# Optimization experiments

Hardware: AMD Instinct MI355X
Metric: run time of the kernel (lower is better)

## Reference

```python
import jax, jax.numpy as jnp
import numpy as np

C = 64

def setup_inputs() -> dict:
    key = jax.random.key(0)
    ks = jax.random.split(key, 8)
    B, H, W = 4, 64, 64
    s = 1.0 / np.sqrt(C)
    return {
        "x": jax.random.normal(ks[0], (B, C, H, W), dtype=jnp.float32),
        "ln_g": jnp.ones((C,), jnp.float32),
        "ln_b": jnp.zeros((C,), jnp.float32),
        "wq": jax.random.normal(ks[1], (C, C), jnp.float32) * s,
        "bq": jnp.zeros((C,), jnp.float32),
        "wk": jax.random.normal(ks[2], (C, 1, 3, 3), jnp.float32) / 3.0,
        "bk": jnp.zeros((C,), jnp.float32),
        "wv": jax.random.normal(ks[3], (C, 1, 3, 3), jnp.float32) / 3.0,
        "bv": jnp.zeros((C,), jnp.float32),
        "wo": jax.random.normal(ks[4], (C, C), jnp.float32) * s,
        "bo": jnp.zeros((C,), jnp.float32),
    }

def _dwconv3x3(x, w, b):
    # depthwise 3x3, padding=1, groups=C; x: (B,C,H,W), w: (C,1,3,3)
    y = jax.lax.conv_general_dilated(
        x, w, window_strides=(1, 1), padding="SAME",
        feature_group_count=x.shape[1],
        dimension_numbers=("NCHW", "OIHW", "NCHW"))
    return y + b[None, :, None, None]

def reference(x, ln_g, ln_b, wq, bq, wk, bk, wv, bv, wo, bo):
    B, Cc, H, W = x.shape
    scale = jnp.sqrt(jnp.asarray(Cc, x.dtype))
    # LayerNorm over channel dim (torch LayerNorm([C]) on (B,H,W,C))
    mu = jnp.mean(x, axis=1, keepdims=True)
    var = jnp.mean(jnp.square(x - mu), axis=1, keepdims=True)
    xn = (x - mu) / jnp.sqrt(var + 1e-5)
    xn = xn * ln_g[None, :, None, None] + ln_b[None, :, None, None]
    # projections
    q = jnp.einsum("oc,bchw->bohw", wq, xn) + bq[None, :, None, None]
    k = _dwconv3x3(xn, wk, bk)
    v = _dwconv3x3(xn, wv, bv)
    HW = H * W
    qf = q.reshape(B, Cc, HW)  # (B,C,N)
    kf = k.reshape(B, Cc, HW)
    vf = v.reshape(B, Cc, HW)
    # attn[b,i,j] = sum_c q[b,c,i] k[b,c,j] / sqrt(C)
    attn = jnp.einsum("bci,bcj->bij", qf, kf) / scale
    attn = jax.nn.softmax(attn, axis=-1)
    # out[b,c,i] = sum_j attn[b,i,j] v[b,c,j]
    out = jnp.einsum("bij,bcj->bci", attn, vf).reshape(B, Cc, H, W)
    out = jnp.einsum("oc,bchw->bohw", wo, out) + bo[None, :, None, None]
    return out + x
```

## Files before the change

kernel.cpp:

```cpp
#include <hip/hip_runtime.h>
#include <stdint.h>

typedef __attribute__((ext_vector_type(8))) short short8;
typedef __attribute__((ext_vector_type(4))) float f32x4;

#define MFMA16(A, B, C) __builtin_amdgcn_mfma_f32_16x16x32_bf16(A, B, C, 0, 0, 0)

__device__ __forceinline__ short f2bf(float f) {
    uint32_t u = __float_as_uint(f);
    u = (u + 0x7fffu + ((u >> 16) & 1u)) >> 16;
    return (short)u;
}
__device__ __forceinline__ float bf2f(short s) {
    return __uint_as_float(((uint32_t)(uint16_t)s) << 16);
}
__device__ __forceinline__ uint32_t pk_bf_trunc(float a, float b) {
    return __builtin_amdgcn_perm(__float_as_uint(b), __float_as_uint(a), 0x07060302u);
}

__device__ __forceinline__ void async_cp16(void* lds, const void* gm) {
    __builtin_amdgcn_global_load_lds(
        (const __attribute__((address_space(1))) unsigned int*)gm,
        (__attribute__((address_space(3))) unsigned int*)lds,
        16, 0, 0);
}

__device__ __forceinline__ int swz(int row, int col) {
    return row * 64 + ((((col >> 3) ^ (row & 7)) << 3) | (col & 7));
}

__device__ __forceinline__ short8 ldg_f8_bf(const float* __restrict__ p) {
    float4 a = *(const float4*)p;
    float4 b = *(const float4*)(p + 4);
    short8 r;
    r[0] = f2bf(a.x); r[1] = f2bf(a.y); r[2] = f2bf(a.z); r[3] = f2bf(a.w);
    r[4] = f2bf(b.x); r[5] = f2bf(b.y); r[6] = f2bf(b.z); r[7] = f2bf(b.w);
    return r;
}

__global__ __launch_bounds__(512, 2) void k_lnqkv(
    const float* __restrict__ xg, const float* __restrict__ lng, const float* __restrict__ lnb,
    const float* __restrict__ wq, const float* __restrict__ bq,
    const float* __restrict__ wkg, const float* __restrict__ bk,
    const float* __restrict__ wvg, const float* __restrict__ bv,
    short* __restrict__ Qt, short* __restrict__ KVg)
{
    const int t    = threadIdx.x;
    const int wv   = t >> 6;
    const int lane = t & 63;
    const int l15  = lane & 15;
    const int quad = lane >> 4;
    const int h    = blockIdx.x;
    const int b    = blockIdx.y;

    __shared__ float xl[3 * 64 * 66];
    __shared__ short sb[64 * 72];
    __shared__ float wkl[576], wvl[576], bkl[64], bvl[64];

    float* muL = (float*)sb;
    float* rsL = muL + 192;

    float rv[24];
    #pragma unroll
    for (int k = 0; k < 24; ++k) {
        int idx = t + (k << 9);
        int dy = idx >> 12, rem = idx & 4095;
        int c = rem >> 6, w = rem & 63;
        int hh = h + dy - 1;
        rv[k] = 0.f;
        if (hh >= 0 && hh < 64) rv[k] = xg[((b * 64 + c) * 64 + hh) * 64 + w];
    }
    for (int idx = t; idx < 576; idx += 512) { wkl[idx] = wkg[idx]; wvl[idx] = wvg[idx]; }
    if (t < 64) { bkl[t] = bk[t]; bvl[t] = bv[t]; }
    #pragma unroll
    for (int k = 0; k < 24; ++k) {
        int idx = t + (k << 9);
        int dy = idx >> 12, rem = idx & 4095;
        int c = rem >> 6, w = rem & 63;
        xl[(dy * 64 + c) * 66 + w] = rv[k];
    }
    __syncthreads();

    if (t < 384) {
        int dy = t >> 7;
        int rem = t & 127;
        int w = rem >> 1, half = rem & 1;
        const float* col = &xl[(dy * 64 + half * 32) * 66 + w];
        float s = 0.f, ss = 0.f;
        #pragma unroll
        for (int cc = 0; cc < 32; ++cc) {
            float v = col[cc * 66];
            s += v; ss = fmaf(v, v, ss);
        }
        s  += __shfl_xor(s, 1);
        ss += __shfl_xor(ss, 1);
        if (half == 0) {
            float mu  = s * (1.f / 64.f);
            float var = ss * (1.f / 64.f) - mu * mu;
            muL[dy * 64 + w] = mu;
            rsL[dy * 64 + w] = rsqrtf(var + 1e-5f);
        }
    }
    __syncthreads();

    #pragma unroll
    for (int k = 0; k < 24; ++k) {
        int idx = t + (k << 9);
        int dy = idx >> 12, rem = idx & 4095;
        int c = rem >> 6, w = rem & 63;
        int hh = h + dy - 1;
        float v = xl[(dy * 64 + c) * 66 + w];
        int p = dy * 64 + w;
        v = (v - muL[p]) * rsL[p] * lng[c] + lnb[c];
        if (hh < 0 || hh >= 64) v = 0.f;
        xl[(dy * 64 + c) * 66 + w] = v;
    }
    __syncthreads();

    {
        short* xnt = sb;
        int c = t & 63;
        #pragma unroll
        for (int k = 0; k < 8; ++k) {
            int w = wv + (k << 3);
            xnt[w * 72 + c] = f2bf(xl[(64 + c) * 66 + w]);
        }
    }
    __syncthreads();

    {
        const short* xnt = sb;
        const int tile = wv >> 1, half = wv & 1;
        short8 af[2];
        #pragma unroll
        for (int kc = 0; kc < 2; ++kc)
            af[kc] = *(const short8*)&xnt[(tile * 16 + l15) * 72 + kc * 32 + quad * 8];
        f32x4 acc[2];
        acc[0] = (f32x4){0.f, 0.f, 0.f, 0.f};
        acc[1] = (f32x4){0.f, 0.f, 0.f, 0.f};
        #pragma unroll
        for (int kc = 0; kc < 2; ++kc) {
            #pragma unroll
            for (int ntl = 0; ntl < 2; ++ntl) {
                int nt = half * 2 + ntl;
                short8 bf = ldg_f8_bf(&wq[(nt * 16 + l15) * 64 + kc * 32 + quad * 8]);
                acc[ntl] = MFMA16(af[kc], bf, acc[ntl]);
            }
        }
        const float c1 = 0.18033688011112042f;
        #pragma unroll
        for (int ntl = 0; ntl < 2; ++ntl) {
            int o = (half * 2 + ntl) * 16 + l15;
            float bqv = bq[o];
            #pragma unroll
            for (int r = 0; r < 4; ++r) {
                int w = tile * 16 + quad * 4 + r;
                Qt[((b * 4096 + h * 64 + w) << 6) + o] = f2bf((acc[ntl][r] + bqv) * c1);
            }
        }
    }
    __syncthreads();

    {
        short* vt = sb;
        int c  = t & 63;
        int w0 = wv << 3;
        float wk9[9], wv9[9];
        #pragma unroll
        for (int q = 0; q < 9; ++q) { wk9[q] = wkl[c * 9 + q]; wv9[q] = wvl[c * 9 + q]; }
        float acck[8], accv[8];
        #pragma unroll
        for (int j = 0; j < 8; ++j) { acck[j] = bkl[c]; accv[j] = bvl[c]; }
        #pragma unroll
        for (int dy = 0; dy < 3; ++dy) {
            const float* row = &xl[(dy * 64 + c) * 66];
            float r[10];
            r[0] = (w0 == 0) ? 0.f : row[w0 - 1];
            #pragma unroll
            for (int j = 0; j < 8; ++j) r[j + 1] = row[w0 + j];
            r[9] = (w0 == 56) ? 0.f : row[w0 + 8];
            #pragma unroll
            for (int j = 0; j < 8; ++j) {
                acck[j] += wk9[0 + dy * 3] * r[j] + wk9[1 + dy * 3] * r[j + 1] + wk9[2 + dy * 3] * r[j + 2];
                accv[j] += wv9[0 + dy * 3] * r[j] + wv9[1 + dy * 3] * r[j + 1] + wv9[2 + dy * 3] * r[j + 2];
            }
        }
        long tb = (long)(b * 64 + h) * 8192;
        #pragma unroll
        for (int j = 0; j < 8; ++j)
            KVg[tb + swz(w0 + j, c)] = f2bf(acck[j]);
        #pragma unroll
        for (int j = 0; j < 8; ++j)
            vt[c * 72 + w0 + j] = f2bf(accv[j]);
    }
    __syncthreads();

    {
        const short* vt = sb;
        long tb = (long)(b * 64 + h) * 8192 + 4096;
        for (int idx = t; idx < 4096; idx += 512) {
            int c = idx >> 6, jl = idx & 63;
            int s = ((jl & 15) << 2) | (jl >> 4);
            KVg[tb + swz(c, s)] = vt[c * 72 + jl];
        }
    }
}

__global__ __launch_bounds__(128, 2) void k_attn(
    const short* __restrict__ Qt, const short* __restrict__ KVg,
    short* __restrict__ Ogb, float* __restrict__ Lg)
{
    const int t    = threadIdx.x;
    const int wv   = t >> 6;
    const int lane = t & 63;
    const int l15  = lane & 15;
    const int quad = lane >> 4;
    const int ti   = blockIdx.x;
    const int jp   = blockIdx.y;
    const int b    = blockIdx.z;
    const int iw   = ti * 64 + wv * 32;

    __shared__ short kvb0[8192];
    __shared__ short kvb1[8192];
    __shared__ short ldsP[2 * 16 * 72];
    short* myP = &ldsP[wv * 16 * 72];

    const short* kvg = KVg + ((long)b * 64 + jp * 16) * 8192;

    short8 qf[2][2];
    #pragma unroll
    for (int rs = 0; rs < 2; ++rs)
        #pragma unroll
        for (int kc = 0; kc < 2; ++kc)
            qf[rs][kc] = *(const short8*)&Qt[((b * 4096 + iw + rs * 16 + l15) << 6) + kc * 32 + quad * 8];

    f32x4 oacc[2][4];
    #pragma unroll
    for (int rs = 0; rs < 2; ++rs)
        #pragma unroll
        for (int nt = 0; nt < 4; ++nt) oacc[rs][nt] = (f32x4){0.f, 0.f, 0.f, 0.f};
    float Lp[2][4] = {{0.f, 0.f, 0.f, 0.f}, {0.f, 0.f, 0.f, 0.f}};

    #pragma unroll
    for (int ii = 0; ii < 8; ++ii) {
        int inst = (wv << 3) + ii;
        async_cp16(kvb0 + inst * 512, kvg + inst * 512 + lane * 8);
    }

    const int xr = l15 & 7;

    #pragma unroll 1
    for (int jt = 0; jt < 16; ++jt) {
        short* cur = (jt & 1) ? kvb1 : kvb0;
        short* nxt = (jt & 1) ? kvb0 : kvb1;
        __syncthreads();
        if (jt < 15) {
            const short* g = kvg + (jt + 1) * 8192;
            #pragma unroll
            for (int ii = 0; ii < 8; ++ii) {
                int inst = (wv << 3) + ii;
                async_cp16(nxt + inst * 512, g + inst * 512 + lane * 8);
            }
        }

        short8 kf[4][2], vf[4][2];
        #pragma unroll
        for (int n = 0; n < 4; ++n) {
            int rbase = (n * 16 + l15) * 64;
            #pragma unroll
            for (int kc = 0; kc < 2; ++kc) {
                int cc = ((kc * 4 + quad) ^ xr) << 3;
                kf[n][kc] = *(const short8*)&cur[rbase + cc];
                vf[n][kc] = *(const short8*)&cur[4096 + rbase + cc];
            }
        }

        #pragma unroll
        for (int rs = 0; rs < 2; ++rs) {
            f32x4 sacc[4];
            #pragma unroll
            for (int n = 0; n < 4; ++n) sacc[n] = (f32x4){0.f, 0.f, 0.f, 0.f};
            #pragma unroll
            for (int kc = 0; kc < 2; ++kc)
                #pragma unroll
                for (int n = 0; n < 4; ++n)
                    sacc[n] = MFMA16(qf[rs][kc], kf[n][kc], sacc[n]);

            #pragma unroll
            for (int r = 0; r < 4; ++r) {
                float p0 = __builtin_amdgcn_exp2f(sacc[0][r]);
                float p1 = __builtin_amdgcn_exp2f(sacc[1][r]);
                float p2 = __builtin_amdgcn_exp2f(sacc[2][r]);
                float p3 = __builtin_amdgcn_exp2f(sacc[3][r]);
                Lp[rs][r] += (p0 + p1) + (p2 + p3);
                uint2 pk;
                pk.x = pk_bf_trunc(p0, p1);
                pk.y = pk_bf_trunc(p2, p3);
                *(uint2*)&myP[(quad * 4 + r) * 72 + l15 * 4] = pk;
            }
            short8 pf[2];
            #pragma unroll
            for (int kc = 0; kc < 2; ++kc)
                pf[kc] = *(const short8*)&myP[l15 * 72 + kc * 32 + quad * 8];
            #pragma unroll
            for (int kc = 0; kc < 2; ++kc)
                #pragma unroll
                for (int n = 0; n < 4; ++n)
                    oacc[rs][n] = MFMA16(pf[kc], vf[n][kc], oacc[rs][n]);
        }
    }

    const int p = b * 4 + jp;
    #pragma unroll
    for (int rs = 0; rs < 2; ++rs) {
        #pragma unroll
        for (int r = 0; r < 4; ++r) {
            #pragma unroll
            for (int off = 1; off < 16; off <<= 1)
                Lp[rs][r] += __shfl_xor(Lp[rs][r], off);
            int i = iw + rs * 16 + quad * 4 + r;
            if (l15 == 0) Lg[p * 4096 + i] = Lp[rs][r];
            #pragma unroll
            for (int nt = 0; nt < 4; ++nt)
                Ogb[((p * 4096 + i) << 6) + nt * 16 + l15] = f2bf(oacc[rs][nt][r]);
        }
    }
}

__global__ __launch_bounds__(256, 4) void k_out(
    const short* __restrict__ Ogb, const float* __restrict__ Lg,
    const float* __restrict__ wo, const float* __restrict__ bo,
    const float* __restrict__ xg, float* __restrict__ out)
{
    const int t    = threadIdx.x;
    const int wv4  = t >> 6;
    const int lane = t & 63;
    const int l15  = lane & 15;
    const int quad = lane >> 4;
    const int i0   = blockIdx.x * 16;
    const int b    = blockIdx.y;

    float Ls = 0.f;
    #pragma unroll
    for (int jp = 0; jp < 4; ++jp) Ls += Lg[(b * 4 + jp) * 4096 + i0 + l15];
    float invL = 1.0f / Ls;

    short8 af[2];
    #pragma unroll
    for (int kc = 0; kc < 2; ++kc)
        af[kc] = ldg_f8_bf(&wo[(wv4 * 16 + l15) * 64 + kc * 32 + quad * 8]);

    f32x4 acc = (f32x4){0.f, 0.f, 0.f, 0.f};
    #pragma unroll
    for (int kc = 0; kc < 2; ++kc) {
        float bs[8] = {0.f, 0.f, 0.f, 0.f, 0.f, 0.f, 0.f, 0.f};
        #pragma unroll
        for (int jp = 0; jp < 4; ++jp) {
            short8 ov = *(const short8*)&Ogb[(((b * 4 + jp) * 4096 + i0 + l15) << 6) + kc * 32 + quad * 8];
            #pragma unroll
            for (int e = 0; e < 8; ++e) bs[e] += bf2f(ov[e]);
        }
        short8 bfr;
        #pragma unroll
        for (int e = 0; e < 8; ++e) bfr[e] = f2bf(bs[e] * invL);
        acc = MFMA16(af[kc], bfr, acc);
    }
    #pragma unroll
    for (int r = 0; r < 4; ++r) {
        int o = wv4 * 16 + quad * 4 + r;
        long obase = ((long)(b * 64 + o)) << 12;
        out[obase + i0 + l15] = acc[r] + bo[o] + xg[obase + i0 + l15];
    }
}

extern "C" void kernel_launch(void* const* d_in, const int* in_sizes, int n_in,
                              void* d_out, int out_size, void* d_ws, size_t ws_size,
                              hipStream_t stream) {
    (void)in_sizes; (void)n_in; (void)out_size; (void)ws_size;
    const float* x   = (const float*)d_in[0];
    const float* lng = (const float*)d_in[1];
    const float* lnb = (const float*)d_in[2];
    const float* wq  = (const float*)d_in[3];
    const float* bq  = (const float*)d_in[4];
    const float* wk  = (const float*)d_in[5];
    const float* bk  = (const float*)d_in[6];
    const float* wvw = (const float*)d_in[7];
    const float* bv  = (const float*)d_in[8];
    const float* wo  = (const float*)d_in[9];
    const float* bo  = (const float*)d_in[10];
    float* out = (float*)d_out;

    short* Qt  = (short*)d_ws;
    short* KVg = Qt + 4 * 4096 * 64;
    short* Ogb = KVg + 4 * 64 * 8192;
    float* Lg  = (float*)(Ogb + 16 * 4096 * 64);

    k_lnqkv<<<dim3(64, 4), 512, 0, stream>>>(x, lng, lnb, wq, bq, wk, bk, wvw, bv, Qt, KVg);
    k_attn<<<dim3(64, 4, 4), 128, 0, stream>>>(Qt, KVg, Ogb, Lg);
    k_out<<<dim3(256, 4), 256, 0, stream>>>(Ogb, Lg, wo, bo, x, out);
}
```

Baseline: 118.8 us.

## Transpose attention MFMA so P stays in registers, double rows per wave

The attention kernel now computes S^T = K·Q^T, so the exponentiated probabilities come out in the register layout needed as the B operand of the PV MFMA. This removes the per-tile LDS round-trip for P. Each wave handles 64 query rows instead of 32, which halves the grid and doubles reuse of each K/V tile loaded into LDS, at the cost of more accumulator registers. The LN/QKV kernel also fuses the LayerNorm statistics into the global load pass, keeps normalized values in registers, and permutes V so its transposed store uses vectorized writes.

```diff
diff --git a/kernel.cpp b/kernel.cpp
--- a/kernel.cpp
+++ b/kernel.cpp
@@ -17,6 +17,7 @@
 __device__ __forceinline__ uint32_t pk_bf_trunc(float a, float b) {
     return __builtin_amdgcn_perm(__float_as_uint(b), __float_as_uint(a), 0x07060302u);
 }
+union PFU { uint32_t u[4]; short8 s; };
 
 __device__ __forceinline__ void async_cp16(void* lds, const void* gm) {
     __builtin_amdgcn_global_load_lds(
@@ -27,6 +28,9 @@
 
 __device__ __forceinline__ int swz(int row, int col) {
     return row * 64 + ((((col >> 3) ^ (row & 7)) << 3) | (col & 7));
+}
+__device__ __forceinline__ int pimap(int j) {
+    return ((j >> 5) << 5) + (((j >> 2) & 3) << 3) + (((j >> 4) & 1) << 2) + (j & 3);
 }
 
 __device__ __forceinline__ short8 ldg_f8_bf(const float* __restrict__ p) {
@@ -52,84 +56,74 @@
     const int quad = lane >> 4;
     const int h    = blockIdx.x;
     const int b    = blockIdx.y;
+    const int w    = t & 63;
+    const int g    = t >> 6;
 
     __shared__ float xl[3 * 64 * 66];
-    __shared__ short sb[64 * 72];
+    __shared__ float sfu[3072];
     __shared__ float wkl[576], wvl[576], bkl[64], bvl[64];
-
-    float* muL = (float*)sb;
-    float* rsL = muL + 192;
+    __shared__ float muL[192], rsL[192];
 
     float rv[24];
+    float s0 = 0.f, s1 = 0.f, s2 = 0.f, q0 = 0.f, q1 = 0.f, q2 = 0.f;
     #pragma unroll
     for (int k = 0; k < 24; ++k) {
-        int idx = t + (k << 9);
-        int dy = idx >> 12, rem = idx & 4095;
-        int c = rem >> 6, w = rem & 63;
-        int hh = h + dy - 1;
-        rv[k] = 0.f;
-        if (hh >= 0 && hh < 64) rv[k] = xg[((b * 64 + c) * 64 + hh) * 64 + w];
-    }
+        const int dy = k >> 3, c = g + 8 * (k & 7);
+        const int hh = h + dy - 1;
+        float v = 0.f;
+        if (hh >= 0 && hh < 64) v = xg[((b * 64 + c) * 64 + hh) * 64 + w];
+        rv[k] = v;
+        if (k < 8)       { s0 += v; q0 = fmaf(v, v, q0); }
+        else if (k < 16) { s1 += v; q1 = fmaf(v, v, q1); }
+        else             { s2 += v; q2 = fmaf(v, v, q2); }
+    }
+    float lngv[8], lnbv[8];
+    #pragma unroll
+    for (int j = 0; j < 8; ++j) { lngv[j] = lng[g + 8 * j]; lnbv[j] = lnb[g + 8 * j]; }
     for (int idx = t; idx < 576; idx += 512) { wkl[idx] = wkg[idx]; wvl[idx] = wvg[idx]; }
     if (t < 64) { bkl[t] = bk[t]; bvl[t] = bv[t]; }
     #pragma unroll
-    for (int k = 0; k < 24; ++k) {
-        int idx = t + (k << 9);
-        int dy = idx >> 12, rem = idx & 4095;
-        int c = rem >> 6, w = rem & 63;
-        xl[(dy * 64 + c) * 66 + w] = rv[k];
-    }
-    __syncthreads();
-
-    if (t < 384) {
-        int dy = t >> 7;
-        int rem = t & 127;
-        int w = rem >> 1, half = rem & 1;
-        const float* col = &xl[(dy * 64 + half * 32) * 66 + w];
-        float s = 0.f, ss = 0.f;
-        #pragma unroll
-        for (int cc = 0; cc < 32; ++cc) {
-            float v = col[cc * 66];
-            s += v; ss = fmaf(v, v, ss);
-        }
-        s  += __shfl_xor(s, 1);
-        ss += __shfl_xor(ss, 1);
-        if (half == 0) {
-            float mu  = s * (1.f / 64.f);
-            float var = ss * (1.f / 64.f) - mu * mu;
-            muL[dy * 64 + w] = mu;
-            rsL[dy * 64 + w] = rsqrtf(var + 1e-5f);
-        }
-    }
-    __syncthreads();
-
-    #pragma unroll
-    for (int k = 0; k < 24; ++k) {
-        int idx = t + (k << 9);
-        int dy = idx >> 12, rem = idx & 4095;
-        int c = rem >> 6, w = rem & 63;
-        int hh = h + dy - 1;
-        float v = xl[(dy * 64 + c) * 66 + w];
-        int p = dy * 64 + w;
-        v = (v - muL[p]) * rsL[p] * lng[c] + lnb[c];
-        if (hh < 0 || hh >= 64) v = 0.f;
-        xl[(dy * 64 + c) * 66 + w] = v;
-    }
-    __syncthreads();
-
+    for (int k = 0; k < 24; ++k)
+        xl[((k >> 3) * 64 + g + 8 * (k & 7)) * 66 + w] = rv[k];
+    sfu[(0 * 8 + g) * 64 + w] = s0; sfu[(1 * 8 + g) * 64 + w] = s1; sfu[(2 * 8 + g) * 64 + w] = s2;
+    sfu[1536 + (0 * 8 + g) * 64 + w] = q0; sfu[1536 + (1 * 8 + g) * 64 + w] = q1; sfu[1536 + (2 * 8 + g) * 64 + w] = q2;
+    __syncthreads();
+
+    if (t < 192) {
+        int dy = t >> 6, ww = t & 63;
+        float S = 0.f, SS = 0.f;
+        #pragma unroll
+        for (int gg = 0; gg < 8; ++gg) {
+            S  += sfu[(dy * 8 + gg) * 64 + ww];
+            SS += sfu[1536 + (dy * 8 + gg) * 64 + ww];
+        }
+        float mu  = S * (1.f / 64.f);
+        float var = SS * (1.f / 64.f) - mu * mu;
+        muL[t] = mu;
+        rsL[t] = rsqrtf(var + 1e-5f);
+    }
+    __syncthreads();
+
+    short* xnt = (short*)sfu;
     {
-        short* xnt = sb;
-        int c = t & 63;
-        #pragma unroll
-        for (int k = 0; k < 8; ++k) {
-            int w = wv + (k << 3);
-            xnt[w * 72 + c] = f2bf(xl[(64 + c) * 66 + w]);
+        float mua = muL[w], rsa = rsL[w];
+        float mub = muL[64 + w], rsb = rsL[64 + w];
+        float muc = muL[128 + w], rsc = rsL[128 + w];
+        #pragma unroll
+        for (int k = 0; k < 24; ++k) {
+            int dy = k >> 3, c = g + 8 * (k & 7);
+            int hh = h + dy - 1;
+            float mu = (k < 8) ? mua : (k < 16) ? mub : muc;
+            float rs = (k < 8) ? rsa : (k < 16) ? rsb : rsc;
+            float v = (rv[k] - mu) * rs * lngv[k & 7] + lnbv[k & 7];
+            if (hh < 0 || hh >= 64) v = 0.f;
+            xl[(dy * 64 + c) * 66 + w] = v;
+            if (dy == 1) xnt[w * 72 + c] = f2bf(v);
         }
     }
     __syncthreads();
 
     {
-        const short* xnt = sb;
         const int tile = wv >> 1, half = wv & 1;
         short8 af[2];
         #pragma unroll
@@ -154,15 +148,15 @@
             float bqv = bq[o];
             #pragma unroll
             for (int r = 0; r < 4; ++r) {
-                int w = tile * 16 + quad * 4 + r;
-                Qt[((b * 4096 + h * 64 + w) << 6) + o] = f2bf((acc[ntl][r] + bqv) * c1);
-            }
-        }
-    }
-    __syncthreads();
-
+                int ww = tile * 16 + quad * 4 + r;
+                Qt[((b * 4096 + h * 64 + ww) << 6) + o] = f2bf((acc[ntl][r] + bqv) * c1);
+            }
+        }
+    }
+    __syncthreads();
+
+    short* vt = (short*)sfu;
     {
-        short* vt = sb;
         int c  = t & 63;
         int w0 = wv << 3;
         float wk9[9], wv9[9];
@@ -177,12 +171,15 @@
             float r[10];
             r[0] = (w0 == 0) ? 0.f : row[w0 - 1];
             #pragma unroll
-            for (int j = 0; j < 8; ++j) r[j + 1] = row[w0 + j];
+            for (int j2 = 0; j2 < 4; ++j2) {
+                float2 p2 = *(const float2*)&row[w0 + j2 * 2];
+                r[1 + j2 * 2] = p2.x; r[2 + j2 * 2] = p2.y;
+            }
             r[9] = (w0 == 56) ? 0.f : row[w0 + 8];
             #pragma unroll
             for (int j = 0; j < 8; ++j) {
-                acck[j] += wk9[0 + dy * 3] * r[j] + wk9[1 + dy * 3] * r[j + 1] + wk9[2 + dy * 3] * r[j + 2];
-                accv[j] += wv9[0 + dy * 3] * r[j] + wv9[1 + dy * 3] * r[j + 1] + wv9[2 + dy * 3] * r[j + 2];
+                acck[j] += wk9[dy * 3] * r[j] + wk9[dy * 3 + 1] * r[j + 1] + wk9[dy * 3 + 2] * r[j + 2];
+                accv[j] += wv9[dy * 3] * r[j] + wv9[dy * 3 + 1] * r[j + 1] + wv9[dy * 3 + 2] * r[j + 2];
             }
         }
         long tb = (long)(b * 64 + h) * 8192;
@@ -191,17 +188,19 @@
             KVg[tb + swz(w0 + j, c)] = f2bf(acck[j]);
         #pragma unroll
         for (int j = 0; j < 8; ++j)
-            vt[c * 72 + w0 + j] = f2bf(accv[j]);
+            vt[c * 68 + pimap(w0 + j)] = f2bf(accv[j]);
     }
     __syncthreads();
 
     {
-        const short* vt = sb;
         long tb = (long)(b * 64 + h) * 8192 + 4096;
-        for (int idx = t; idx < 4096; idx += 512) {
-            int c = idx >> 6, jl = idx & 63;
-            int s = ((jl & 15) << 2) | (jl >> 4);
-            KVg[tb + swz(c, s)] = vt[c * 72 + jl];
+        #pragma unroll
+        for (int it = 0; it < 2; ++it) {
+            int grp = t + it * 512;
+            int c = grp >> 4, s0c = (grp & 15) * 4;
+            uint2 v = *(const uint2*)&vt[c * 68 + s0c];
+            int dst = c * 64 + ((((s0c >> 3) ^ (c & 7)) << 3) | (s0c & 7));
+            *(uint2*)&KVg[tb + dst] = v;
         }
     }
 }
@@ -218,34 +217,30 @@
     const int ti   = blockIdx.x;
     const int jp   = blockIdx.y;
     const int b    = blockIdx.z;
-    const int iw   = ti * 64 + wv * 32;
+    const int iw   = ti * 128 + wv * 64;
 
     __shared__ short kvb0[8192];
     __shared__ short kvb1[8192];
-    __shared__ short ldsP[2 * 16 * 72];
-    short* myP = &ldsP[wv * 16 * 72];
 
     const short* kvg = KVg + ((long)b * 64 + jp * 16) * 8192;
 
-    short8 qf[2][2];
-    #pragma unroll
-    for (int rs = 0; rs < 2; ++rs)
+    short8 qf[4][2];
+    #pragma unroll
+    for (int rs = 0; rs < 4; ++rs)
         #pragma unroll
         for (int kc = 0; kc < 2; ++kc)
             qf[rs][kc] = *(const short8*)&Qt[((b * 4096 + iw + rs * 16 + l15) << 6) + kc * 32 + quad * 8];
 
-    f32x4 oacc[2][4];
-    #pragma unroll
-    for (int rs = 0; rs < 2; ++rs)
-        #pragma unroll
-        for (int nt = 0; nt < 4; ++nt) oacc[rs][nt] = (f32x4){0.f, 0.f, 0.f, 0.f};
-    float Lp[2][4] = {{0.f, 0.f, 0.f, 0.f}, {0.f, 0.f, 0.f, 0.f}};
-
-    #pragma unroll
-    for (int ii = 0; ii < 8; ++ii) {
-        int inst = (wv << 3) + ii;
-        async_cp16(kvb0 + inst * 512, kvg + inst * 512 + lane * 8);
-    }
+    f32x4 oacc[4][4];
+    #pragma unroll
+    for (int rs = 0; rs < 4; ++rs)
+        #pragma unroll
+        for (int cb = 0; cb < 4; ++cb) oacc[rs][cb] = (f32x4){0.f, 0.f, 0.f, 0.f};
+    float Lp[4] = {0.f, 0.f, 0.f, 0.f};
+
+    #pragma unroll
+    for (int ii = 0; ii < 8; ++ii)
+        async_cp16(kvb0 + (wv * 8 + ii) * 512, kvg + (wv * 8 + ii) * 512 + lane * 8);
 
     const int xr = l15 & 7;
 
@@ -255,74 +250,68 @@
         short* nxt = (jt & 1) ? kvb0 : kvb1;
         __syncthreads();
         if (jt < 15) {
-            const short* g = kvg + (jt + 1) * 8192;
-            #pragma unroll
-            for (int ii = 0; ii < 8; ++ii) {
-                int inst = (wv << 3) + ii;
-                async_cp16(nxt + inst * 512, g + inst * 512 + lane * 8);
-            }
+            const short* gsrc = kvg + (jt + 1) * 8192;
+            #pragma unroll
+            for (int ii = 0; ii < 8; ++ii)
+                async_cp16(nxt + (wv * 8 + ii) * 512, gsrc + (wv * 8 + ii) * 512 + lane * 8);
         }
 
         short8 kf[4][2], vf[4][2];
         #pragma unroll
-        for (int n = 0; n < 4; ++n) {
-            int rbase = (n * 16 + l15) * 64;
+        for (int mb = 0; mb < 4; ++mb) {
+            int rbase = (mb * 16 + l15) * 64;
             #pragma unroll
             for (int kc = 0; kc < 2; ++kc) {
                 int cc = ((kc * 4 + quad) ^ xr) << 3;
-                kf[n][kc] = *(const short8*)&cur[rbase + cc];
-                vf[n][kc] = *(const short8*)&cur[4096 + rbase + cc];
-            }
-        }
-
-        #pragma unroll
-        for (int rs = 0; rs < 2; ++rs) {
+                kf[mb][kc] = *(const short8*)&cur[rbase + cc];
+                vf[mb][kc] = *(const short8*)&cur[4096 + rbase + cc];
+            }
+        }
+
+        #pragma unroll
+        for (int rs = 0; rs < 4; ++rs) {
             f32x4 sacc[4];
             #pragma unroll
-            for (int n = 0; n < 4; ++n) sacc[n] = (f32x4){0.f, 0.f, 0.f, 0.f};
+            for (int mb = 0; mb < 4; ++mb) sacc[mb] = (f32x4){0.f, 0.f, 0.f, 0.f};
             #pragma unroll
             for (int kc = 0; kc < 2; ++kc)
                 #pragma unroll
-                for (int n = 0; n < 4; ++n)
-                    sacc[n] = MFMA16(qf[rs][kc], kf[n][kc], sacc[n]);
-
-            #pragma unroll
-            for (int r = 0; r < 4; ++r) {
-                float p0 = __builtin_amdgcn_exp2f(sacc[0][r]);
-                float p1 = __builtin_amdgcn_exp2f(sacc[1][r]);
-                float p2 = __builtin_amdgcn_exp2f(sacc[2][r]);
-                float p3 = __builtin_amdgcn_exp2f(sacc[3][r]);
-                Lp[rs][r] += (p0 + p1) + (p2 + p3);
-                uint2 pk;
-                pk.x = pk_bf_trunc(p0, p1);
-                pk.y = pk_bf_trunc(p2, p3);
-                *(uint2*)&myP[(quad * 4 + r) * 72 + l15 * 4] = pk;
-            }
-            short8 pf[2];
-            #pragma unroll
-            for (int kc = 0; kc < 2; ++kc)
-                pf[kc] = *(const short8*)&myP[l15 * 72 + kc * 32 + quad * 8];
-            #pragma unroll
-            for (int kc = 0; kc < 2; ++kc)
+                for (int mb = 0; mb < 4; ++mb)
+                    sacc[mb] = MFMA16(kf[mb][kc], qf[rs][kc], sacc[mb]);
+
+            PFU pf[2];
+            #pragma unroll
+            for (int mb = 0; mb < 4; ++mb) {
+                float p0 = __builtin_amdgcn_exp2f(sacc[mb][0]);
+                float p1 = __builtin_amdgcn_exp2f(sacc[mb][1]);
+                float p2 = __builtin_amdgcn_exp2f(sacc[mb][2]);
+                float p3 = __builtin_amdgcn_exp2f(sacc[mb][3]);
+                Lp[rs] += (p0 + p1) + (p2 + p3);
+                pf[mb >> 1].u[(mb & 1) * 2 + 0] = pk_bf_trunc(p0, p1);
+                pf[mb >> 1].u[(mb & 1) * 2 + 1] = pk_bf_trunc(p2, p3);
+            }
+            #pragma unroll
+            for (int kcp = 0; kcp < 2; ++kcp)
                 #pragma unroll
-                for (int n = 0; n < 4; ++n)
-                    oacc[rs][n] = MFMA16(pf[kc], vf[n][kc], oacc[rs][n]);
+                for (int cb = 0; cb < 4; ++cb)
+                    oacc[rs][cb] = MFMA16(vf[cb][kcp], pf[kcp].s, oacc[rs][cb]);
         }
     }
 
     const int p = b * 4 + jp;
     #pragma unroll
-    for (int rs = 0; rs < 2; ++rs) {
-        #pragma unroll
-        for (int r = 0; r < 4; ++r) {
-            #pragma unroll
-            for (int off = 1; off < 16; off <<= 1)
-                Lp[rs][r] += __shfl_xor(Lp[rs][r], off);
-            int i = iw + rs * 16 + quad * 4 + r;
-            if (l15 == 0) Lg[p * 4096 + i] = Lp[rs][r];
-            #pragma unroll
-            for (int nt = 0; nt < 4; ++nt)
-                Ogb[((p * 4096 + i) << 6) + nt * 16 + l15] = f2bf(oacc[rs][nt][r]);
+    for (int rs = 0; rs < 4; ++rs) {
+        float L = Lp[rs];
+        L += __shfl_xor(L, 16);
+        L += __shfl_xor(L, 32);
+        int i = iw + rs * 16 + l15;
+        if (quad == 0) Lg[p * 4096 + i] = L;
+        #pragma unroll
+        for (int cb = 0; cb < 4; ++cb) {
+            uint2 pk;
+            pk.x = ((uint32_t)(uint16_t)f2bf(oacc[rs][cb][1]) << 16) | (uint16_t)f2bf(oacc[rs][cb][0]);
+            pk.y = ((uint32_t)(uint16_t)f2bf(oacc[rs][cb][3]) << 16) | (uint16_t)f2bf(oacc[rs][cb][2]);
+            *(uint2*)&Ogb[((p * 4096 + i) << 6) + cb * 16 + quad * 4] = pk;
         }
     }
 }
@@ -396,6 +385,6 @@
     float* Lg  = (float*)(Ogb + 16 * 4096 * 64);
 
     k_lnqkv<<<dim3(64, 4), 512, 0, stream>>>(x, lng, lnb, wq, bq, wk, bk, wvw, bv, Qt, KVg);
-    k_attn<<<dim3(64, 4, 4), 128, 0, stream>>>(Qt, KVg, Ogb, Lg);
+    k_attn<<<dim3(32, 4, 4), 128, 0, stream>>>(Qt, KVg, Ogb, Lg);
     k_out<<<dim3(256, 4), 256, 0, stream>>>(Ogb, Lg, wo, bo, x, out);
 }
```

Measured after the change: 123.3 us. 3.8% more time.
